# Optimization experiments

Measured on AMD Instinct MI355X. Metric: run time of the kernel, lower is better.

## Reference

```python
import jax, jax.numpy as jnp
import numpy as np

D_MODEL = 1024
D_HEAD = 64


def setup_inputs() -> dict:
    key = jax.random.key(0)
    k_x, k_q, k_k, k_v, k_o = jax.random.split(key, 5)
    scale = 1.0 / np.sqrt(D_MODEL)
    residual_stream = jax.random.normal(k_x, (4, 2048, D_MODEL), dtype=jnp.float32)
    Q = scale * jax.random.normal(k_q, (D_MODEL, D_HEAD), dtype=jnp.float32)
    K = scale * jax.random.normal(k_k, (D_MODEL, D_HEAD), dtype=jnp.float32)
    V = scale * jax.random.normal(k_v, (D_MODEL, D_HEAD), dtype=jnp.float32)
    O = scale * jax.random.normal(k_o, (D_MODEL, D_HEAD), dtype=jnp.float32)
    return {"residual_stream": residual_stream, "Q": Q, "K": K, "V": V, "O": O}


def reference(residual_stream, Q, K, V, O) -> jnp.ndarray:
    # queries/keys: [B, S, d_head]
    queries = jnp.einsum('bsd,dh->bsh', residual_stream, Q)
    keys = jnp.einsum('bsd,dh->bsh', residual_stream, K)
    # NOTE: original module applies NO 1/sqrt(d_head) scaling.
    pre_attention = jnp.einsum('bqh,bkh->bqk', queries, keys)  # [B, S, S]
    S = pre_attention.shape[-1]
    causal = jnp.tril(jnp.ones((S, S), dtype=bool))
    pre_attention = jnp.where(causal[None], pre_attention, -jnp.inf)
    attention = jax.nn.softmax(pre_attention, axis=-1)
    # x = residual @ V @ O^T : [B, S, d_model]
    x = jnp.einsum('bsd,dh,eh->bse', residual_stream, V, O)
    return jnp.einsum('bqk,bke->bqe', attention, x)
```

## Files before the change

### kernel.cpp

```cpp
#include <hip/hip_runtime.h>
#include <hip/hip_bf16.h>
#include <math.h>

#define BATCH 4
#define SEQ   2048
#define DM    1024
#define DH    64
#define NROWS (BATCH*SEQ)
#define PVSPLIT 8

typedef __hip_bfloat16 bf16;
typedef __attribute__((ext_vector_type(8))) short short8;
typedef __attribute__((ext_vector_type(8))) unsigned short ushortx8;
typedef __attribute__((ext_vector_type(4))) float floatx4;

__device__ __forceinline__ ushort f2bf(float f) {
    union { bf16 h; ushort u; } cv;
    cv.h = __float2bfloat16(f);
    return cv.u;
}
__device__ __forceinline__ float bf2f(ushort u) {
    union { unsigned int i; float f; } v; v.i = ((unsigned int)u) << 16; return v.f;
}

__device__ __forceinline__ void load_lds16(const ushort* g, ushort* l) {
    __builtin_amdgcn_global_load_lds(
        (const __attribute__((address_space(1))) unsigned int*)g,
        (__attribute__((address_space(3))) unsigned int*)l, 16, 0, 0);
}

__global__ __launch_bounds__(256) void wprep_kernel(
    const float* __restrict__ Q, const float* __restrict__ K,
    const float* __restrict__ V, ushort* __restrict__ WhT, ushort* __restrict__ WlT)
{
    int n = blockIdx.x;
    const float* W = (n < 64) ? Q : (n < 128) ? K : V;
    int c = n & 63;
    for (int k = threadIdx.x; k < DM; k += 256) {
        float w = W[k * DH + c];
        ushort hi = f2bf(w);
        WhT[n * DM + k] = hi;
        WlT[n * DM + k] = f2bf(w - bf2f(hi));
    }
}

__global__ __launch_bounds__(256) void qkv_part_kernel(
    const float* __restrict__ x, const ushort* __restrict__ WhT,
    const ushort* __restrict__ WlT, float* __restrict__ Cpart)
{
    __shared__ __align__(16) ushort Xs[2][32][34];
    __shared__ __align__(16) ushort Ws[2][192][34];
    int s0 = blockIdx.x * 32;
    int kb = blockIdx.y * 256;
    int t = threadIdx.x;
    int wave = t >> 6, lane = t & 63, m_ = lane & 15, qd = lane >> 4;
    const floatx4 z4 = {0.f, 0.f, 0.f, 0.f};
    floatx4 accq[2] = {z4, z4}, acck[2] = {z4, z4}, accv[2] = {z4, z4};
    int xr = t >> 3, xc = (t & 7) * 4;
    for (int k0 = 0; k0 < 256; k0 += 32) {
        float4 v = *(const float4*)&x[(size_t)(s0 + xr) * DM + kb + k0 + xc];
        ushort h0 = f2bf(v.x), h1 = f2bf(v.y), h2 = f2bf(v.z), h3 = f2bf(v.w);
        *(ushort4*)&Xs[0][xr][xc] = make_ushort4(h0, h1, h2, h3);
        *(ushort4*)&Xs[1][xr][xc] = make_ushort4(
            f2bf(v.x - bf2f(h0)), f2bf(v.y - bf2f(h1)),
            f2bf(v.z - bf2f(h2)), f2bf(v.w - bf2f(h3)));
        #pragma unroll
        for (int j = 0; j < 3; ++j) {
            int idx = t + j * 256, n = idx >> 2, kc = (idx & 3) * 8;
            *(uint4*)&Ws[0][n][kc] = *(const uint4*)&WhT[n * DM + kb + k0 + kc];
            *(uint4*)&Ws[1][n][kc] = *(const uint4*)&WlT[n * DM + kb + k0 + kc];
        }
        __syncthreads();
        short8 ah[2], al[2];
        #pragma unroll
        for (int mi = 0; mi < 2; ++mi) {
            ah[mi] = *(const short8*)&Xs[0][mi * 16 + m_][qd * 8];
            al[mi] = *(const short8*)&Xs[1][mi * 16 + m_][qd * 8];
        }
        int nq = wave * 16 + m_, nk = 64 + wave * 16 + m_, nv = 128 + wave * 16 + m_;
        short8 bqh = *(const short8*)&Ws[0][nq][qd * 8];
        short8 bql = *(const short8*)&Ws[1][nq][qd * 8];
        short8 bkh = *(const short8*)&Ws[0][nk][qd * 8];
        short8 bkl = *(const short8*)&Ws[1][nk][qd * 8];
        short8 bvh = *(const short8*)&Ws[0][nv][qd * 8];
        #pragma unroll
        for (int mi = 0; mi < 2; ++mi) {
            accq[mi] = __builtin_amdgcn_mfma_f32_16x16x32_bf16(ah[mi], bqh, accq[mi], 0, 0, 0);
            accq[mi] = __builtin_amdgcn_mfma_f32_16x16x32_bf16(al[mi], bqh, accq[mi], 0, 0, 0);
            accq[mi] = __builtin_amdgcn_mfma_f32_16x16x32_bf16(ah[mi], bql, accq[mi], 0, 0, 0);
            acck[mi] = __builtin_amdgcn_mfma_f32_16x16x32_bf16(ah[mi], bkh, acck[mi], 0, 0, 0);
            acck[mi] = __builtin_amdgcn_mfma_f32_16x16x32_bf16(al[mi], bkh, acck[mi], 0, 0, 0);
            acck[mi] = __builtin_amdgcn_mfma_f32_16x16x32_bf16(ah[mi], bkl, acck[mi], 0, 0, 0);
            accv[mi] = __builtin_amdgcn_mfma_f32_16x16x32_bf16(ah[mi], bvh, accv[mi], 0, 0, 0);
        }
        __syncthreads();
    }
    float* Cp = Cpart + (size_t)blockIdx.y * (NROWS * 192);
    #pragma unroll
    for (int mi = 0; mi < 2; ++mi) {
        #pragma unroll
        for (int r = 0; r < 4; ++r) {
            int row = s0 + mi * 16 + qd * 4 + r;
            float* base = Cp + (size_t)row * 192;
            base[wave * 16 + m_]       = accq[mi][r];
            base[64 + wave * 16 + m_]  = acck[mi][r];
            base[128 + wave * 16 + m_] = accv[mi][r];
        }
    }
}

__global__ __launch_bounds__(256) void qkv_reduce_kernel(
    const float* __restrict__ Cpart,
    ushort* __restrict__ qh, ushort* __restrict__ ql,
    ushort* __restrict__ kh, ushort* __restrict__ kl, ushort* __restrict__ xvhT)
{
    __shared__ ushort xvs[32][72];
    const size_t SL = (size_t)NROWS * 192;
    int row0 = blockIdx.x * 32;
    int t = threadIdx.x;
    #pragma unroll
    for (int i = 0; i < 24; ++i) {
        int e = i * 256 + t;
        int r = e / 192, c = e - r * 192;
        size_t row = row0 + r;
        size_t off = row * 192 + c;
        float s = Cpart[off] + Cpart[SL + off] + Cpart[2 * SL + off] + Cpart[3 * SL + off];
        ushort hi = f2bf(s);
        if (c < 64) {
            qh[row * 64 + c] = hi; ql[row * 64 + c] = f2bf(s - bf2f(hi));
        } else if (c < 128) {
            kh[row * 64 + c - 64] = hi; kl[row * 64 + c - 64] = f2bf(s - bf2f(hi));
        } else {
            xvs[r][c - 128] = hi;
        }
    }
    __syncthreads();
    int h = t >> 2, seg = t & 3;
    ushortx8 v;
    #pragma unroll
    for (int k = 0; k < 8; ++k) v[k] = xvs[seg * 8 + k][h];
    int b = row0 >> 11, sl = row0 & 2047;
    *(ushortx8*)&xvhT[(((size_t)(b * 64 + h)) << 11) + sl + seg * 8] = v;
}

__global__ __launch_bounds__(256) void softmax_kernel(
    const ushort* __restrict__ qh, const ushort* __restrict__ ql,
    const ushort* __restrict__ kh, const ushort* __restrict__ kl,
    ushort* __restrict__ P, float* __restrict__ lpart)
{
    __shared__ __align__(16) ushort Qs[2][2][32][72];
    __shared__ float lred[4][2][32];
    int pp = blockIdx.x & 31, b = blockIdx.x >> 5, s = blockIdx.y;
    int jA = pp, jB = 63 - pp;
    int srowA = jA << 5, srowB = jB << 5;
    int s0gA = (b << 11) + srowA, s0gB = (b << 11) + srowB;
    int t = threadIdx.x, wave = t >> 6, lane = t & 63, m_ = lane & 15, qd = lane >> 4;
    #pragma unroll
    for (int i = 0; i < 4; ++i) {
        int idx = i * 256 + t;
        int tile = idx >> 9, hl = (idx >> 8) & 1, r = (idx >> 3) & 31, c = (idx & 7) * 8;
        const ushort* src = (hl ? ql : qh) + (size_t)((tile ? s0gB : s0gA) + r) * 64 + c;
        *(uint4*)&Qs[tile][hl][r][c] = *(const uint4*)src;
    }
    __syncthreads();
    const ushort* khb = kh + ((size_t)b << 11) * 64;
    const ushort* klb = kl + ((size_t)b << 11) * 64;
    int ntA = (jA >> 1) + 1, ntB = (jB >> 1) + 1;
    int nAs = (ntA > s) ? (((ntA - 1 - s) >> 2) + 1) : 0;
    int nBs = (ntB > s) ? (((ntB - 1 - s) >> 2) + 1) : 0;
    int ntot = nAs + nBs;
    const floatx4 z4 = {0.f, 0.f, 0.f, 0.f};
    float llA[2][4] = {{0.f,0.f,0.f,0.f},{0.f,0.f,0.f,0.f}};
    float llB[2][4] = {{0.f,0.f,0.f,0.f},{0.f,0.f,0.f,0.f}};
    for (int it = wave; it < ntot; it += 4) {
        int isA = (it < nAs);
        int ti = isA ? (s + 4 * it) : (s + 4 * (it - nAs));
        int srow = isA ? srowA : srowB;
        int s0g = isA ? s0gA : s0gB;
        int tidx = isA ? 0 : 1;
        int k0 = ti << 6;
        floatx4 acc[2][4];
        #pragma unroll
        for (int mi = 0; mi < 2; ++mi)
            #pragma unroll
            for (int ni = 0; ni < 4; ++ni) acc[mi][ni] = z4;
        #pragma unroll
        for (int kk = 0; kk < 2; ++kk) {
            short8 ah0 = *(const short8*)&Qs[tidx][0][0 * 16 + m_][kk * 32 + qd * 8];
            short8 ah1 = *(const short8*)&Qs[tidx][0][1 * 16 + m_][kk * 32 + qd * 8];
            short8 al0 = *(const short8*)&Qs[tidx][1][0 * 16 + m_][kk * 32 + qd * 8];
            short8 al1 = *(const short8*)&Qs[tidx][1][1 * 16 + m_][kk * 32 + qd * 8];
            #pragma unroll
            for (int ni = 0; ni < 4; ++ni) {
                size_t koff = (size_t)(k0 + ni * 16 + m_) * 64 + kk * 32 + qd * 8;
                short8 bh = *(const short8*)&khb[koff];
                short8 bl = *(const short8*)&klb[koff];
                acc[0][ni] = __builtin_amdgcn_mfma_f32_16x16x32_bf16(ah0, bh, acc[0][ni], 0, 0, 0);
                acc[0][ni] = __builtin_amdgcn_mfma_f32_16x16x32_bf16(al0, bh, acc[0][ni], 0, 0, 0);
                acc[0][ni] = __builtin_amdgcn_mfma_f32_16x16x32_bf16(ah0, bl, acc[0][ni], 0, 0, 0);
                acc[1][ni] = __builtin_amdgcn_mfma_f32_16x16x32_bf16(ah1, bh, acc[1][ni], 0, 0, 0);
                acc[1][ni] = __builtin_amdgcn_mfma_f32_16x16x32_bf16(al1, bh, acc[1][ni], 0, 0, 0);
                acc[1][ni] = __builtin_amdgcn_mfma_f32_16x16x32_bf16(ah1, bl, acc[1][ni], 0, 0, 0);
            }
        }
        #pragma unroll
        for (int mi = 0; mi < 2; ++mi)
            #pragma unroll
            for (int ni = 0; ni < 4; ++ni) {
                int kc = k0 + ni * 16 + m_;
                #pragma unroll
                for (int r = 0; r < 4; ++r) {
                    int row = srow + mi * 16 + qd * 4 + r;
                    float p = (kc <= row) ? __expf(acc[mi][ni][r]) : 0.f;
                    if (isA) llA[mi][r] += p; else llB[mi][r] += p;
                    P[(size_t)(s0g + mi * 16 + qd * 4 + r) * 2048 + kc] = f2bf(p);
                }
            }
    }
    #pragma unroll
    for (int d = 1; d < 16; d <<= 1)
        #pragma unroll
        for (int mi = 0; mi < 2; ++mi)
            #pragma unroll
            for (int r = 0; r < 4; ++r) {
                llA[mi][r] += __shfl_xor(llA[mi][r], d);
                llB[mi][r] += __shfl_xor(llB[mi][r], d);
            }
    if (m_ == 0)
        #pragma unroll
        for (int mi = 0; mi < 2; ++mi)
            #pragma unroll
            for (int r = 0; r < 4; ++r) {
                lred[wave][0][mi * 16 + qd * 4 + r] = llA[mi][r];
                lred[wave][1][mi * 16 + qd * 4 + r] = llB[mi][r];
            }
    __syncthreads();
    if (t < 64) {
        int tile = t >> 5, row = t & 31;
        float sm = lred[0][tile][row] + lred[1][tile][row]
                 + lred[2][tile][row] + lred[3][tile][row];
        lpart[(size_t)s * NROWS + (tile ? s0gB : s0gA) + row] = sm;
    }
}

__global__ __launch_bounds__(256) void pv_kernel(
    const ushort* __restrict__ P, const ushort* __restrict__ xvhT,
    float* __restrict__ AxvPart)
{
    __shared__ __align__(16) ushort AL[2][64 * 64];
    __shared__ __align__(16) ushort AS[2][64 * 64];
    __shared__ __align__(16) ushort Bs[2][64 * 64];
    int bid = blockIdx.x;
    int p = bid >> 5;
    int b = (bid >> 3) & 3;
    int s = bid & 7;
    int m0L = (31 - p) << 6, m0S = p << 6;
    int ntL = 32 - p, ntS = p + 1;
    int nL = (ntL - s + 7) >> 3;
    int nS = (ntS > s) ? ((ntS - s + 7) >> 3) : 0;
    int t = threadIdx.x, wave = t >> 6, lane = t & 63, m_ = lane & 15, qd = lane >> 4;
    const ushort* Pb = P + ((size_t)b << 22);
    const ushort* Xb = xvhT + ((size_t)(b * 64) << 11);
    const floatx4 z4 = {0.f, 0.f, 0.f, 0.f};
    floatx4 accL[2][2], accS[2][2];
    #pragma unroll
    for (int mi = 0; mi < 2; ++mi)
        #pragma unroll
        for (int ni = 0; ni < 2; ++ni) { accL[mi][ni] = z4; accS[mi][ni] = z4; }
    int mb = (wave >> 1) << 5;
    int nb = (wave & 1) << 5;
    int drow = lane >> 3;
    int dlc = ((lane & 7) ^ drow) << 3;
    #define PV_STAGE(tt, buf)                                                    \
        {                                                                        \
            int k0_ = (s + 8 * (tt)) << 6;                                       \
            _Pragma("unroll")                                                    \
            for (int i_ = 0; i_ < 6; ++i_) {                                     \
                int c_ = wave * 6 + i_;                                          \
                if (c_ < 8)                                                      \
                    load_lds16(Pb + (size_t)(m0L + c_ * 8 + drow) * SEQ + k0_ + dlc, \
                               &AL[buf][c_ * 512]);                              \
                else if (c_ < 16)                                                \
                    load_lds16(Xb + (size_t)((c_ - 8) * 8 + drow) * SEQ + k0_ + dlc, \
                               &Bs[buf][(c_ - 8) * 512]);                        \
                else if ((tt) < nS)                                              \
                    load_lds16(Pb + (size_t)(m0S + (c_ - 16) * 8 + drow) * SEQ + k0_ + dlc, \
                               &AS[buf][(c_ - 16) * 512]);                       \
            }                                                                    \
        }
    PV_STAGE(0, 0)
    for (int tt = 0; tt < nL; ++tt) {
        __syncthreads();
        if (tt + 1 < nL) PV_STAGE(tt + 1, (tt + 1) & 1)
        int bufi = tt & 1;
        #pragma unroll
        for (int kk = 0; kk < 2; ++kk) {
            short8 bb[2];
            #pragma unroll
            for (int ni = 0; ni < 2; ++ni) {
                int row = nb + ni * 16 + m_;
                bb[ni] = *(const short8*)&Bs[bufi][row * 64 + (((kk << 2) + qd) ^ (row & 7)) * 8];
            }
            #pragma unroll
            for (int mi = 0; mi < 2; ++mi) {
                int row = mb + mi * 16 + m_;
                short8 aL = *(const short8*)&AL[bufi][row * 64 + (((kk << 2) + qd) ^ (row & 7)) * 8];
                #pragma unroll
                for (int ni = 0; ni < 2; ++ni)
                    accL[mi][ni] = __builtin_amdgcn_mfma_f32_16x16x32_bf16(aL, bb[ni], accL[mi][ni], 0, 0, 0);
            }
            if (tt < nS) {
                #pragma unroll
                for (int mi = 0; mi < 2; ++mi) {
                    int row = mb + mi * 16 + m_;
                    short8 aS = *(const short8*)&AS[bufi][row * 64 + (((kk << 2) + qd) ^ (row & 7)) * 8];
                    #pragma unroll
                    for (int ni = 0; ni < 2; ++ni)
                        accS[mi][ni] = __builtin_amdgcn_mfma_f32_16x16x32_bf16(aS, bb[ni], accS[mi][ni], 0, 0, 0);
                }
            }
        }
    }
    float* Ap = AxvPart + (size_t)s * (NROWS * DH);
    #pragma unroll
    for (int mi = 0; mi < 2; ++mi) {
        #pragma unroll
        for (int r = 0; r < 4; ++r) {
            int rowL = m0L + mb + mi * 16 + qd * 4 + r;
            int rowS = m0S + mb + mi * 16 + qd * 4 + r;
            float* orL = Ap + (size_t)((b << 11) + rowL) * DH + nb;
            float* orS = Ap + (size_t)((b << 11) + rowS) * DH + nb;
            #pragma unroll
            for (int ni = 0; ni < 2; ++ni) {
                orL[ni * 16 + m_] = accL[mi][ni][r];
                orS[ni * 16 + m_] = accS[mi][ni][r];
            }
        }
    }
    #undef PV_STAGE
}

__global__ __launch_bounds__(256) void out_kernel(
    const float* __restrict__ AxvPart, const float* __restrict__ lpart,
    const float* __restrict__ O, float* __restrict__ out)
{
    __shared__ __align__(16) ushort As[2][64][72];
    __shared__ __align__(16) ushort Bsh[2][128][72];
    __shared__ float lsc[64];
    int bid = blockIdx.x;
    int r0 = (bid >> 3) << 6;
    int e0 = (bid & 7) << 7;
    int t = threadIdx.x;
    if (t < 64) {
        int rg = r0 + t;
        lsc[t] = 1.f / (lpart[rg] + lpart[NROWS + rg]
                      + lpart[2 * NROWS + rg] + lpart[3 * NROWS + rg]);
    }
    __syncthreads();
    const size_t PSL = (size_t)NROWS * DH;
    #pragma unroll
    for (int i = 0; i < 16; ++i) {
        int idx = i * 256 + t;
        int r = idx >> 6, h = idx & 63;
        size_t off = (size_t)(r0 + r) * DH + h;
        float a = 0.f;
        #pragma unroll
        for (int sp = 0; sp < PVSPLIT; ++sp) a += AxvPart[sp * PSL + off];
        a *= lsc[r];
        ushort hi = f2bf(a);
        As[0][r][h] = hi;
        As[1][r][h] = f2bf(a - bf2f(hi));
    }
    #pragma unroll
    for (int i = 0; i < 32; ++i) {
        int idx = i * 256 + t;
        int r = idx >> 6, h = idx & 63;
        float w = O[(size_t)(e0 + r) * DH + h];
        ushort hi = f2bf(w);
        Bsh[0][r][h] = hi;
        Bsh[1][r][h] = f2bf(w - bf2f(hi));
    }
    __syncthreads();
    int wave = t >> 6, lane = t & 63, m_ = lane & 15, qd = lane >> 4;
    const floatx4 z4 = {0.f, 0.f, 0.f, 0.f};
    floatx4 acc[8] = {z4, z4, z4, z4, z4, z4, z4, z4};
    #pragma unroll
    for (int kk = 0; kk < 2; ++kk) {
        short8 ah = *(const short8*)&As[0][wave * 16 + m_][kk * 32 + qd * 8];
        short8 al = *(const short8*)&As[1][wave * 16 + m_][kk * 32 + qd * 8];
        #pragma unroll
        for (int ni = 0; ni < 8; ++ni) {
            short8 bh = *(const short8*)&Bsh[0][ni * 16 + m_][kk * 32 + qd * 8];
            short8 bl = *(const short8*)&Bsh[1][ni * 16 + m_][kk * 32 + qd * 8];
            acc[ni] = __builtin_amdgcn_mfma_f32_16x16x32_bf16(ah, bh, acc[ni], 0, 0, 0);
            acc[ni] = __builtin_amdgcn_mfma_f32_16x16x32_bf16(al, bh, acc[ni], 0, 0, 0);
            acc[ni] = __builtin_amdgcn_mfma_f32_16x16x32_bf16(ah, bl, acc[ni], 0, 0, 0);
        }
    }
    #pragma unroll
    for (int r = 0; r < 4; ++r) {
        int row = r0 + wave * 16 + qd * 4 + r;
        float* orow = out + (size_t)row * DM + e0;
        #pragma unroll
        for (int ni = 0; ni < 8; ++ni)
            orow[ni * 16 + m_] = acc[ni][r];
    }
}

extern "C" void kernel_launch(void* const* d_in, const int* in_sizes, int n_in,
                              void* d_out, int out_size, void* d_ws, size_t ws_size,
                              hipStream_t stream) {
    const float* x = (const float*)d_in[0];
    const float* Q = (const float*)d_in[1];
    const float* K = (const float*)d_in[2];
    const float* V = (const float*)d_in[3];
    const float* O = (const float*)d_in[4];
    float* out = (float*)d_out;

    char* ws = (char*)d_ws;
    ushort* qh   = (ushort*)(ws);
    ushort* ql   = (ushort*)(ws + (1ull  << 20));
    ushort* kh   = (ushort*)(ws + (2ull  << 20));
    ushort* kl   = (ushort*)(ws + (3ull  << 20));
    ushort* xvhT = (ushort*)(ws + (4ull  << 20));
    ushort* WhT  = (ushort*)(ws + (5ull  << 20));
    ushort* WlT  = (ushort*)(ws + (5ull  << 20) + (512ull << 10));
    float*  lpart = (float*)(ws + (6ull  << 20));
    float*  AxvPart = (float*)(ws + (7ull << 20));
    ushort* Pbuf = (ushort*)(ws + (23ull << 20));
    float*  Cpart = (float*)(ws + (23ull << 20));

    wprep_kernel<<<192, 256, 0, stream>>>(Q, K, V, WhT, WlT);
    qkv_part_kernel<<<dim3(NROWS / 32, 4), 256, 0, stream>>>(x, WhT, WlT, Cpart);
    qkv_reduce_kernel<<<NROWS / 32, 256, 0, stream>>>(Cpart, qh, ql, kh, kl, xvhT);
    softmax_kernel<<<dim3(32 * BATCH, 4), 256, 0, stream>>>(qh, ql, kh, kl, Pbuf, lpart);
    pv_kernel<<<16 * 4 * PVSPLIT, 256, 0, stream>>>(Pbuf, xvhT, AxvPart);
    out_kernel<<<(NROWS / 64) * 8, 256, 0, stream>>>(AxvPart, lpart, O, out);
}
```

Measured before the change: 181.6 us.

## Hoist split-K reduction and O bf16 split out of out_kernel

```diff
diff --git a/kernel.cpp b/kernel.cpp
--- a/kernel.cpp
+++ b/kernel.cpp
@@ -31,16 +31,29 @@
 
 __global__ __launch_bounds__(256) void wprep_kernel(
     const float* __restrict__ Q, const float* __restrict__ K,
-    const float* __restrict__ V, ushort* __restrict__ WhT, ushort* __restrict__ WlT)
+    const float* __restrict__ V, const float* __restrict__ O,
+    ushort* __restrict__ WhT, ushort* __restrict__ WlT,
+    ushort* __restrict__ Oh, ushort* __restrict__ Ol)
 {
     int n = blockIdx.x;
-    const float* W = (n < 64) ? Q : (n < 128) ? K : V;
-    int c = n & 63;
-    for (int k = threadIdx.x; k < DM; k += 256) {
-        float w = W[k * DH + c];
-        ushort hi = f2bf(w);
-        WhT[n * DM + k] = hi;
-        WlT[n * DM + k] = f2bf(w - bf2f(hi));
+    if (n < 192) {
+        const float* W = (n < 64) ? Q : (n < 128) ? K : V;
+        int c = n & 63;
+        for (int k = threadIdx.x; k < DM; k += 256) {
+            float w = W[k * DH + c];
+            ushort hi = f2bf(w);
+            WhT[n * DM + k] = hi;
+            WlT[n * DM + k] = f2bf(w - bf2f(hi));
+        }
+    } else {
+        int e0 = (n - 192) << 4;
+        for (int idx = threadIdx.x; idx < 16 * DH; idx += 256) {
+            int off = (e0 << 6) + idx;
+            float w = O[off];
+            ushort hi = f2bf(w);
+            Oh[off] = hi;
+            Ol[off] = f2bf(w - bf2f(hi));
+        }
     }
 }
 
@@ -340,45 +353,62 @@
     #undef PV_STAGE
 }
 
+__global__ __launch_bounds__(256) void axv_reduce_kernel(
+    const float* __restrict__ AxvPart, const float* __restrict__ lpart,
+    ushort* __restrict__ Axvh, ushort* __restrict__ Axvl)
+{
+    const size_t PSL = (size_t)NROWS * DH;
+    int idx = blockIdx.x * 256 + threadIdx.x;
+    size_t e = (size_t)idx * 4;
+    int r = (int)(e >> 6);
+    float4 a = *(const float4*)&AxvPart[e];
+    #pragma unroll
+    for (int sp = 1; sp < PVSPLIT; ++sp) {
+        float4 v = *(const float4*)&AxvPart[sp * PSL + e];
+        a.x += v.x; a.y += v.y; a.z += v.z; a.w += v.w;
+    }
+    float sc = 1.f / (lpart[r] + lpart[NROWS + r]
+                    + lpart[2 * NROWS + r] + lpart[3 * NROWS + r]);
+    a.x *= sc; a.y *= sc; a.z *= sc; a.w *= sc;
+    ushort h0 = f2bf(a.x), h1 = f2bf(a.y), h2 = f2bf(a.z), h3 = f2bf(a.w);
+    *(ushort4*)&Axvh[e] = make_ushort4(h0, h1, h2, h3);
+    *(ushort4*)&Axvl[e] = make_ushort4(
+        f2bf(a.x - bf2f(h0)), f2bf(a.y - bf2f(h1)),
+        f2bf(a.z - bf2f(h2)), f2bf(a.w - bf2f(h3)));
+}
+
 __global__ __launch_bounds__(256) void out_kernel(
-    const float* __restrict__ AxvPart, const float* __restrict__ lpart,
-    const float* __restrict__ O, float* __restrict__ out)
+    const ushort* __restrict__ Axvh, const ushort* __restrict__ Axvl,
+    const ushort* __restrict__ Oh, const ushort* __restrict__ Ol,
+    float* __restrict__ out)
 {
     __shared__ __align__(16) ushort As[2][64][72];
     __shared__ __align__(16) ushort Bsh[2][128][72];
-    __shared__ float lsc[64];
     int bid = blockIdx.x;
     int r0 = (bid >> 3) << 6;
     int e0 = (bid & 7) << 7;
     int t = threadIdx.x;
-    if (t < 64) {
-        int rg = r0 + t;
-        lsc[t] = 1.f / (lpart[rg] + lpart[NROWS + rg]
-                      + lpart[2 * NROWS + rg] + lpart[3 * NROWS + rg]);
-    }
-    __syncthreads();
-    const size_t PSL = (size_t)NROWS * DH;
-    #pragma unroll
-    for (int i = 0; i < 16; ++i) {
-        int idx = i * 256 + t;
-        int r = idx >> 6, h = idx & 63;
-        size_t off = (size_t)(r0 + r) * DH + h;
-        float a = 0.f;
-        #pragma unroll
-        for (int sp = 0; sp < PVSPLIT; ++sp) a += AxvPart[sp * PSL + off];
-        a *= lsc[r];
-        ushort hi = f2bf(a);
-        As[0][r][h] = hi;
-        As[1][r][h] = f2bf(a - bf2f(hi));
-    }
-    #pragma unroll
-    for (int i = 0; i < 32; ++i) {
-        int idx = i * 256 + t;
-        int r = idx >> 6, h = idx & 63;
-        float w = O[(size_t)(e0 + r) * DH + h];
-        ushort hi = f2bf(w);
-        Bsh[0][r][h] = hi;
-        Bsh[1][r][h] = f2bf(w - bf2f(hi));
+    {
+        int tr = t >> 2, tc = (t & 3) << 4;
+        const ushort* ah = Axvh + (size_t)(r0 + tr) * DH + tc;
+        const ushort* al = Axvl + (size_t)(r0 + tr) * DH + tc;
+        *(uint4*)&As[0][tr][tc]     = *(const uint4*)ah;
+        *(uint4*)&As[0][tr][tc + 8] = *(const uint4*)(ah + 8);
+        *(uint4*)&As[1][tr][tc]     = *(const uint4*)al;
+        *(uint4*)&As[1][tr][tc + 8] = *(const uint4*)(al + 8);
+    }
+    {
+        int tr = t >> 1, tc = (t & 1) << 5;
+        const ushort* bh = Oh + (size_t)(e0 + tr) * DH + tc;
+        const ushort* bl = Ol + (size_t)(e0 + tr) * DH + tc;
+        *(uint4*)&Bsh[0][tr][tc]      = *(const uint4*)bh;
+        *(uint4*)&Bsh[0][tr][tc + 8]  = *(const uint4*)(bh + 8);
+        *(uint4*)&Bsh[0][tr][tc + 16] = *(const uint4*)(bh + 16);
+        *(uint4*)&Bsh[0][tr][tc + 24] = *(const uint4*)(bh + 24);
+        *(uint4*)&Bsh[1][tr][tc]      = *(const uint4*)bl;
+        *(uint4*)&Bsh[1][tr][tc + 8]  = *(const uint4*)(bl + 8);
+        *(uint4*)&Bsh[1][tr][tc + 16] = *(const uint4*)(bl + 16);
+        *(uint4*)&Bsh[1][tr][tc + 24] = *(const uint4*)(bl + 24);
     }
     __syncthreads();
     int wave = t >> 6, lane = t & 63, m_ = lane & 15, qd = lane >> 4;
@@ -426,14 +456,19 @@
     ushort* WhT  = (ushort*)(ws + (5ull  << 20));
     ushort* WlT  = (ushort*)(ws + (5ull  << 20) + (512ull << 10));
     float*  lpart = (float*)(ws + (6ull  << 20));
+    ushort* Oh   = (ushort*)(ws + (6ull  << 20) + (256ull << 10));
+    ushort* Ol   = (ushort*)(ws + (6ull  << 20) + (384ull << 10));
     float*  AxvPart = (float*)(ws + (7ull << 20));
     ushort* Pbuf = (ushort*)(ws + (23ull << 20));
     float*  Cpart = (float*)(ws + (23ull << 20));
-
-    wprep_kernel<<<192, 256, 0, stream>>>(Q, K, V, WhT, WlT);
+    ushort* Axvh = qh;
+    ushort* Axvl = ql;
+
+    wprep_kernel<<<256, 256, 0, stream>>>(Q, K, V, O, WhT, WlT, Oh, Ol);
     qkv_part_kernel<<<dim3(NROWS / 32, 4), 256, 0, stream>>>(x, WhT, WlT, Cpart);
     qkv_reduce_kernel<<<NROWS / 32, 256, 0, stream>>>(Cpart, qh, ql, kh, kl, xvhT);
     softmax_kernel<<<dim3(32 * BATCH, 4), 256, 0, stream>>>(qh, ql, kh, kl, Pbuf, lpart);
     pv_kernel<<<16 * 4 * PVSPLIT, 256, 0, stream>>>(Pbuf, xvhT, AxvPart);
-    out_kernel<<<(NROWS / 64) * 8, 256, 0, stream>>>(AxvPart, lpart, O, out);
-}
+    axv_reduce_kernel<<<NROWS * DH / 4 / 256, 256, 0, stream>>>(AxvPart, lpart, Axvh, Axvl);
+    out_kernel<<<(NROWS / 64) * 8, 256, 0, stream>>>(Axvh, Axvl, Oh, Ol, out);
+}
```

Result: faster. 162.1 us (-10.8%).
